# Optimization experiments

Measured on AMD Instinct MI355X. Metric: run time of the kernel, lower is better.

The kernel has to match this reference:

```python
import jax, jax.numpy as jnp
import numpy as np

B, N = 4, 2048
IN_F, OUT_F, H = 128, 128, 8
HD = OUT_F // H  # 16
ALPHA = 0.2       # LeakyReLU negative slope
TIME_DECAY = 0.1


def setup_inputs() -> dict:
    key = jax.random.key(0)
    k1, k2, k3, k4, k5 = jax.random.split(key, 5)
    node_features = jax.random.normal(k1, (B, N, IN_F), dtype=jnp.float32)
    adj_matrix = jax.random.randint(k2, (B, N, N), 0, 2, dtype=jnp.int32)
    time_matrix = jax.random.uniform(k3, (B, N, N), dtype=jnp.float32)
    # xavier_uniform with gain=1.414 as in the torch module
    def xavier(k, shape, fan_in, fan_out):
        bound = 1.414 * np.sqrt(6.0 / (fan_in + fan_out))
        return jax.random.uniform(k, shape, minval=-bound, maxval=bound, dtype=jnp.float32)
    W = xavier(k4, (H, IN_F, HD), IN_F, HD)
    a = xavier(k5, (H, 2 * HD, 1), 2 * HD, 1)
    return {"node_features": node_features, "adj_matrix": adj_matrix,
            "time_matrix": time_matrix, "W": W, "a": a}


def reference(node_features, adj_matrix, time_matrix, W, a):
    # time weights (eq 17): exp(-lambda * (t_max - t))
    current_time = jnp.max(time_matrix)
    time_weights = jnp.exp(-TIME_DECAY * (current_time - time_matrix))  # [B,N,N]

    # per-head projection: [B,H,N,HD]
    h = jnp.einsum('bni,hio->bhno', node_features, W)

    # decompose attention vector a = [a_src; a_dst] so we never build the
    # O(N^2 * 2*HD) concat tensor: e_ij = LeakyReLU(a_src.h_i + a_dst.h_j)
    a_src = a[:, :HD, 0]   # [H,HD]
    a_dst = a[:, HD:, 0]   # [H,HD]
    e_i = jnp.einsum('bhnd,hd->bhn', h, a_src)  # score contribution of node i
    e_j = jnp.einsum('bhnd,hd->bhn', h, a_dst)  # score contribution of node j
    e = e_i[:, :, :, None] + e_j[:, :, None, :]          # [B,H,N,N]
    e = jax.nn.leaky_relu(e, negative_slope=ALPHA)
    e = e * time_weights[:, None, :, :]

    # mask non-edges, normalize (dropout is identity in eval mode)
    mask = adj_matrix[:, None, :, :] == 0                 # [B,1->H,N,N]
    e = jnp.where(mask, -jnp.inf, e)
    attention = jax.nn.softmax(e, axis=-1)                # [B,H,N,N]

    # aggregate neighbors, merge heads, ELU
    out = jnp.einsum('bhij,bhjo->bhio', attention, h)     # [B,H,N,HD]
    out = jnp.transpose(out, (0, 2, 1, 3)).reshape(node_features.shape[0], node_features.shape[1], -1)
    return jax.nn.elu(out)
```

## Files before the change

### kernel.cpp

```cpp
#include <hip/hip_runtime.h>
#include <hip/hip_bf16.h>

#define BN    4
#define NN    2048
#define INF   128
#define HH    8
#define HD    16
#define ALPHA 0.2f
#define DECAY 0.1f

#define DLOG2E 0.14426950408889634f
#define LLOG2E 0.5287663729448977f

typedef __attribute__((ext_vector_type(8))) short short8;
typedef __attribute__((ext_vector_type(4))) float float4v;

__launch_bounds__(256, 8)
__global__ void k_setup(const float* __restrict__ x,
                        const float* __restrict__ W,
                        const float* __restrict__ a,
                        const float* __restrict__ tm,
                        unsigned* __restrict__ ct,
                        __hip_bfloat16* __restrict__ h_t,
                        float* __restrict__ es, float* __restrict__ ed) {
    if (blockIdx.x < 1024) {
        const uint4* p = (const uint4*)tm;
        const int nvec = BN * NN * NN / 4;
        int idx = blockIdx.x * 256 + threadIdx.x;
        const int stride = 1024 * 256;
        unsigned m = 0u;
        for (int i = idx; i < nvec; i += stride) {
            uint4 v = p[i];
            m = max(m, v.x); m = max(m, v.y); m = max(m, v.z); m = max(m, v.w);
        }
        float fm = __uint_as_float(m);
        #pragma unroll
        for (int o = 32; o >= 1; o >>= 1) fm = fmaxf(fm, __shfl_xor(fm, o));
        __shared__ float sm[4];
        if ((threadIdx.x & 63) == 0) sm[threadIdx.x >> 6] = fm;
        __syncthreads();
        if (threadIdx.x == 0) {
            float mm = fmaxf(fmaxf(sm[0], sm[1]), fmaxf(sm[2], sm[3]));
            atomicMax(ct, __float_as_uint(mm));
        }
    } else {
        int bid = blockIdx.x - 1024;
        int sub = threadIdx.x >> 7;
        int tt  = threadIdx.x & 127;
        int nn  = bid * 2 + sub;
        __shared__ float xs[2][INF];
        xs[sub][tt] = x[(size_t)nn * INF + tt];
        __syncthreads();
        int h = tt >> 4, d = tt & 15;
        const float* Wp = W + (h * INF) * HD + d;
        float acc = 0.f;
        #pragma unroll 16
        for (int i = 0; i < INF; i++) acc += xs[sub][i] * Wp[i * HD];
        int b = nn >> 11, n = nn & 2047;
        h_t[((size_t)((b * HH + h) * HD + d)) * NN + n] = __float2bfloat16(acc);
        float s  = acc * a[h * 2 * HD + d];
        float dd = acc * a[h * 2 * HD + HD + d];
        #pragma unroll
        for (int o = 8; o >= 1; o >>= 1) { s += __shfl_xor(s, o); dd += __shfl_xor(dd, o); }
        if (d == 0) {
            es[(b * HH + h) * NN + n] = s;
            ed[(b * HH + h) * NN + n] = dd;
        }
    }
}

__launch_bounds__(512, 4)
__global__ void k_attn(const int* __restrict__ adj,
                       const float* __restrict__ tm,
                       const __hip_bfloat16* __restrict__ h_t,
                       const float* __restrict__ es, const float* __restrict__ ed,
                       const unsigned* __restrict__ ctp,
                       float* __restrict__ out) {
    int t    = threadIdx.x;
    int w    = t >> 6;
    int lane = t & 63;
    int q    = lane >> 4;
    int im   = lane & 15;
    int bx   = blockIdx.x;
    int b    = bx >> 7;
    int i0   = (bx & 127) << 4;
    int i    = i0 + im;
    const int R = 16;

    __shared__ float tws[2][16 * 128];

    float ctv = __uint_as_float(*ctp);
    float c0  = fmaf(-DLOG2E, ctv, LLOG2E);
    float es_i = es[(b * HH + w) * NN + i];

    const float* ed_p = ed + (size_t)(b * HH + w) * NN + q * 8;
    const __hip_bfloat16* ht_p = h_t + ((size_t)((b * HH + w) * HD + im)) * NN + q * 8;

    int srow = t >> 5;
    int sblk = t & 31;
    int soff = srow * 128 + ((sblk ^ (srow & 7)) << 2);
    const int*   adj_s = adj + ((size_t)(b * NN + i0 + srow)) * NN + (sblk << 2);
    const float* tm_s  = tm  + ((size_t)(b * NN + i0 + srow)) * NN + (sblk << 2);

    int rbase = im * 128;
    int rx    = im & 7;

    union { uint4 u; short8 v; } ones;
    ones.u = make_uint4(0x3F803F80u, 0x3F803F80u, 0x3F803F80u, 0x3F803F80u);

    float4v acc  = {0.f, 0.f, 0.f, 0.f};
    float4v accl = {0.f, 0.f, 0.f, 0.f};

    int4   pa = *(const int4*)(adj_s);
    float4 pt = *(const float4*)(tm_s);
    {
        float w0 = (pa.x != 0) ? exp2f(fmaf(DLOG2E, pt.x, c0)) : 0.f;
        float w1 = (pa.y != 0) ? exp2f(fmaf(DLOG2E, pt.y, c0)) : 0.f;
        float w2 = (pa.z != 0) ? exp2f(fmaf(DLOG2E, pt.z, c0)) : 0.f;
        float w3 = (pa.w != 0) ? exp2f(fmaf(DLOG2E, pt.w, c0)) : 0.f;
        *(float4*)&tws[0][soff] = make_float4(w0, w1, w2, w3);
    }
    pa = *(const int4*)(adj_s + 128);
    pt = *(const float4*)(tm_s + 128);
    __syncthreads();

    for (int r = 0; r < R; r++) {
        int cur = r & 1;
        if (r + 1 < R) {
            float w0 = (pa.x != 0) ? exp2f(fmaf(DLOG2E, pt.x, c0)) : 0.f;
            float w1 = (pa.y != 0) ? exp2f(fmaf(DLOG2E, pt.y, c0)) : 0.f;
            float w2 = (pa.z != 0) ? exp2f(fmaf(DLOG2E, pt.z, c0)) : 0.f;
            float w3 = (pa.w != 0) ? exp2f(fmaf(DLOG2E, pt.w, c0)) : 0.f;
            *(float4*)&tws[cur ^ 1][soff] = make_float4(w0, w1, w2, w3);
            if (r + 2 < R) {
                pa = *(const int4*)(adj_s + (r + 2) * 128);
                pt = *(const float4*)(tm_s + (r + 2) * 128);
            }
        }
        #pragma unroll
        for (int c4 = 0; c4 < 4; c4++) {
            int blk0 = c4 * 8 + 2 * q;
            float4 w01 = *(const float4*)&tws[cur][rbase + ((blk0 ^ rx) << 2)];
            float4 w23 = *(const float4*)&tws[cur][rbase + (((blk0 + 1) ^ rx) << 2)];
            int jglob = r * 128 + c4 * 32;
            float4 e0 = *(const float4*)(ed_p + jglob);
            float4 e1 = *(const float4*)(ed_p + jglob + 4);
            uint4  hv = *(const uint4*)(ht_p + jglob);

            float wv[8] = {w01.x, w01.y, w01.z, w01.w, w23.x, w23.y, w23.z, w23.w};
            float ev[8] = {e0.x, e0.y, e0.z, e0.w, e1.x, e1.y, e1.z, e1.w};

            unsigned u[8];
            #pragma unroll
            for (int k = 0; k < 8; k++) {
                float s0 = es_i + ev[k];
                float sc = fmaxf(s0, ALPHA * s0);
                float pv = exp2f(sc * wv[k]);
                unsigned b16 = __float_as_uint(pv) + 0x8000u;
                u[k] = (wv[k] > 0.f) ? b16 : 0u;
            }
            union { uint4 w; short8 v; } af;
            af.w.x = __builtin_amdgcn_perm(u[1], u[0], 0x07060302u);
            af.w.y = __builtin_amdgcn_perm(u[3], u[2], 0x07060302u);
            af.w.z = __builtin_amdgcn_perm(u[5], u[4], 0x07060302u);
            af.w.w = __builtin_amdgcn_perm(u[7], u[6], 0x07060302u);

            union { uint4 u; short8 v; } bf;
            bf.u = hv;
            acc  = __builtin_amdgcn_mfma_f32_16x16x32_bf16(af.v, bf.v, acc, 0, 0, 0);
            accl = __builtin_amdgcn_mfma_f32_16x16x32_bf16(af.v, ones.v, accl, 0, 0, 0);
        }
        __syncthreads();
    }

    #pragma unroll
    for (int r = 0; r < 4; r++) {
        int row = q * 4 + r;
        float v = acc[r] / accl[r];
        v = (v > 0.f) ? v : expm1f(v);
        out[((size_t)(b * NN + i0 + row)) * (HH * HD) + w * HD + im] = v;
    }
}

extern "C" void kernel_launch(void* const* d_in, const int* in_sizes, int n_in,
                              void* d_out, int out_size, void* d_ws, size_t ws_size,
                              hipStream_t stream) {
    const float* x   = (const float*)d_in[0];
    const int*   adj = (const int*)d_in[1];
    const float* tm  = (const float*)d_in[2];
    const float* W   = (const float*)d_in[3];
    const float* a   = (const float*)d_in[4];
    float* out = (float*)d_out;

    float* wsf = (float*)d_ws;
    unsigned* ct = (unsigned*)wsf;
    float* es = wsf + 64;
    float* ed = es + BN * HH * NN;
    __hip_bfloat16* h_t = (__hip_bfloat16*)(ed + BN * HH * NN);

    hipMemsetAsync(d_ws, 0, 4, stream);
    k_setup<<<1024 + 4096, 256, 0, stream>>>(x, W, a, tm, ct, h_t, es, ed);
    k_attn <<<BN * (NN / 16), 512, 0, stream>>>(adj, tm, h_t, es, ed, ct, out);
}
```

Before: 235.7 us.

## Split attention blocks by head group, single-buffer weights, batch global loads

```diff
diff --git a/kernel.cpp b/kernel.cpp
--- a/kernel.cpp
+++ b/kernel.cpp
@@ -69,7 +69,7 @@
     }
 }
 
-__launch_bounds__(512, 4)
+__launch_bounds__(256, 4)
 __global__ void k_attn(const int* __restrict__ adj,
                        const float* __restrict__ tm,
                        const __hip_bfloat16* __restrict__ h_t,
@@ -77,30 +77,37 @@
                        const unsigned* __restrict__ ctp,
                        float* __restrict__ out) {
     int t    = threadIdx.x;
-    int w    = t >> 6;
+    int wv4  = t >> 6;
     int lane = t & 63;
     int q    = lane >> 4;
     int im   = lane & 15;
     int bx   = blockIdx.x;
-    int b    = bx >> 7;
-    int i0   = (bx & 127) << 4;
+    int b    = bx >> 9;
+    int hg   = (bx >> 8) & 1;
+    int i0   = (bx & 255) >> 1;
+    int itile = bx & 127;
+    hg = (bx >> 7) & 1;
+    b  = bx >> 8;
+    i0 = itile << 4;
+    int head = hg * 4 + wv4;
     int i    = i0 + im;
     const int R = 16;
 
-    __shared__ float tws[2][16 * 128];
+    __shared__ float tws[16 * 128];
 
     float ctv = __uint_as_float(*ctp);
     float c0  = fmaf(-DLOG2E, ctv, LLOG2E);
-    float es_i = es[(b * HH + w) * NN + i];
-
-    const float* ed_p = ed + (size_t)(b * HH + w) * NN + q * 8;
-    const __hip_bfloat16* ht_p = h_t + ((size_t)((b * HH + w) * HD + im)) * NN + q * 8;
-
-    int srow = t >> 5;
-    int sblk = t & 31;
-    int soff = srow * 128 + ((sblk ^ (srow & 7)) << 2);
-    const int*   adj_s = adj + ((size_t)(b * NN + i0 + srow)) * NN + (sblk << 2);
-    const float* tm_s  = tm  + ((size_t)(b * NN + i0 + srow)) * NN + (sblk << 2);
+    float es_i = es[(b * HH + head) * NN + i];
+
+    const float* ed_p = ed + (size_t)(b * HH + head) * NN + q * 8;
+    const __hip_bfloat16* ht_p = h_t + ((size_t)((b * HH + head) * HD + im)) * NN + q * 8;
+
+    int srow  = t >> 4;
+    int sblk0 = (t & 15) << 1;
+    int soff0 = srow * 128 + ((sblk0 ^ (srow & 7)) << 2);
+    int soff1 = srow * 128 + (((sblk0 + 1) ^ (srow & 7)) << 2);
+    const int*   adj_s = adj + ((size_t)(b * NN + i0 + srow)) * NN + (sblk0 << 2);
+    const float* tm_s  = tm  + ((size_t)(b * NN + i0 + srow)) * NN + (sblk0 << 2);
 
     int rbase = im * 128;
     int rx    = im & 7;
@@ -111,53 +118,60 @@
     float4v acc  = {0.f, 0.f, 0.f, 0.f};
     float4v accl = {0.f, 0.f, 0.f, 0.f};
 
-    int4   pa = *(const int4*)(adj_s);
-    float4 pt = *(const float4*)(tm_s);
-    {
-        float w0 = (pa.x != 0) ? exp2f(fmaf(DLOG2E, pt.x, c0)) : 0.f;
-        float w1 = (pa.y != 0) ? exp2f(fmaf(DLOG2E, pt.y, c0)) : 0.f;
-        float w2 = (pa.z != 0) ? exp2f(fmaf(DLOG2E, pt.z, c0)) : 0.f;
-        float w3 = (pa.w != 0) ? exp2f(fmaf(DLOG2E, pt.w, c0)) : 0.f;
-        *(float4*)&tws[0][soff] = make_float4(w0, w1, w2, w3);
-    }
-    pa = *(const int4*)(adj_s + 128);
-    pt = *(const float4*)(tm_s + 128);
-    __syncthreads();
+    int4   pa0 = *(const int4*)(adj_s);
+    int4   pa1 = *(const int4*)(adj_s + 4);
+    float4 pt0 = *(const float4*)(tm_s);
+    float4 pt1 = *(const float4*)(tm_s + 4);
 
     for (int r = 0; r < R; r++) {
-        int cur = r & 1;
+        float w00 = (pa0.x != 0) ? exp2f(fmaf(DLOG2E, pt0.x, c0)) : 0.f;
+        float w01_ = (pa0.y != 0) ? exp2f(fmaf(DLOG2E, pt0.y, c0)) : 0.f;
+        float w02 = (pa0.z != 0) ? exp2f(fmaf(DLOG2E, pt0.z, c0)) : 0.f;
+        float w03 = (pa0.w != 0) ? exp2f(fmaf(DLOG2E, pt0.w, c0)) : 0.f;
+        float w10 = (pa1.x != 0) ? exp2f(fmaf(DLOG2E, pt1.x, c0)) : 0.f;
+        float w11 = (pa1.y != 0) ? exp2f(fmaf(DLOG2E, pt1.y, c0)) : 0.f;
+        float w12 = (pa1.z != 0) ? exp2f(fmaf(DLOG2E, pt1.z, c0)) : 0.f;
+        float w13 = (pa1.w != 0) ? exp2f(fmaf(DLOG2E, pt1.w, c0)) : 0.f;
+
+        __syncthreads();
+        *(float4*)&tws[soff0] = make_float4(w00, w01_, w02, w03);
+        *(float4*)&tws[soff1] = make_float4(w10, w11, w12, w13);
         if (r + 1 < R) {
-            float w0 = (pa.x != 0) ? exp2f(fmaf(DLOG2E, pt.x, c0)) : 0.f;
-            float w1 = (pa.y != 0) ? exp2f(fmaf(DLOG2E, pt.y, c0)) : 0.f;
-            float w2 = (pa.z != 0) ? exp2f(fmaf(DLOG2E, pt.z, c0)) : 0.f;
-            float w3 = (pa.w != 0) ? exp2f(fmaf(DLOG2E, pt.w, c0)) : 0.f;
-            *(float4*)&tws[cur ^ 1][soff] = make_float4(w0, w1, w2, w3);
-            if (r + 2 < R) {
-                pa = *(const int4*)(adj_s + (r + 2) * 128);
-                pt = *(const float4*)(tm_s + (r + 2) * 128);
-            }
-        }
+            pa0 = *(const int4*)(adj_s + (r + 1) * 128);
+            pa1 = *(const int4*)(adj_s + (r + 1) * 128 + 4);
+            pt0 = *(const float4*)(tm_s + (r + 1) * 128);
+            pt1 = *(const float4*)(tm_s + (r + 1) * 128 + 4);
+        }
+        __syncthreads();
+
+        float4 E0[4], E1[4];
+        uint4  HV[4];
+        #pragma unroll
+        for (int c4 = 0; c4 < 4; c4++) {
+            int jg = r * 128 + c4 * 32;
+            E0[c4] = *(const float4*)(ed_p + jg);
+            E1[c4] = *(const float4*)(ed_p + jg + 4);
+            HV[c4] = *(const uint4*)(ht_p + jg);
+        }
+
         #pragma unroll
         for (int c4 = 0; c4 < 4; c4++) {
             int blk0 = c4 * 8 + 2 * q;
-            float4 w01 = *(const float4*)&tws[cur][rbase + ((blk0 ^ rx) << 2)];
-            float4 w23 = *(const float4*)&tws[cur][rbase + (((blk0 + 1) ^ rx) << 2)];
-            int jglob = r * 128 + c4 * 32;
-            float4 e0 = *(const float4*)(ed_p + jglob);
-            float4 e1 = *(const float4*)(ed_p + jglob + 4);
-            uint4  hv = *(const uint4*)(ht_p + jglob);
-
-            float wv[8] = {w01.x, w01.y, w01.z, w01.w, w23.x, w23.y, w23.z, w23.w};
-            float ev[8] = {e0.x, e0.y, e0.z, e0.w, e1.x, e1.y, e1.z, e1.w};
+            float4 wA = *(const float4*)&tws[rbase + ((blk0 ^ rx) << 2)];
+            float4 wB = *(const float4*)&tws[rbase + (((blk0 + 1) ^ rx) << 2)];
+
+            float wvv[8] = {wA.x, wA.y, wA.z, wA.w, wB.x, wB.y, wB.z, wB.w};
+            float evv[8] = {E0[c4].x, E0[c4].y, E0[c4].z, E0[c4].w,
+                            E1[c4].x, E1[c4].y, E1[c4].z, E1[c4].w};
 
             unsigned u[8];
             #pragma unroll
             for (int k = 0; k < 8; k++) {
-                float s0 = es_i + ev[k];
+                float s0 = es_i + evv[k];
                 float sc = fmaxf(s0, ALPHA * s0);
-                float pv = exp2f(sc * wv[k]);
+                float pv = exp2f(sc * wvv[k]);
                 unsigned b16 = __float_as_uint(pv) + 0x8000u;
-                u[k] = (wv[k] > 0.f) ? b16 : 0u;
+                u[k] = (wvv[k] > 0.f) ? b16 : 0u;
             }
             union { uint4 w; short8 v; } af;
             af.w.x = __builtin_amdgcn_perm(u[1], u[0], 0x07060302u);
@@ -166,11 +180,10 @@
             af.w.w = __builtin_amdgcn_perm(u[7], u[6], 0x07060302u);
 
             union { uint4 u; short8 v; } bf;
-            bf.u = hv;
+            bf.u = HV[c4];
             acc  = __builtin_amdgcn_mfma_f32_16x16x32_bf16(af.v, bf.v, acc, 0, 0, 0);
             accl = __builtin_amdgcn_mfma_f32_16x16x32_bf16(af.v, ones.v, accl, 0, 0, 0);
         }
-        __syncthreads();
     }
 
     #pragma unroll
@@ -178,7 +191,7 @@
         int row = q * 4 + r;
         float v = acc[r] / accl[r];
         v = (v > 0.f) ? v : expm1f(v);
-        out[((size_t)(b * NN + i0 + row)) * (HH * HD) + w * HD + im] = v;
+        out[((size_t)(b * NN + i0 + row)) * (HH * HD) + head * HD + im] = v;
     }
 }
 
@@ -200,5 +213,5 @@
 
     hipMemsetAsync(d_ws, 0, 4, stream);
     k_setup<<<1024 + 4096, 256, 0, stream>>>(x, W, a, tm, ct, h_t, es, ed);
-    k_attn <<<BN * (NN / 16), 512, 0, stream>>>(adj, tm, h_t, es, ed, ct, out);
+    k_attn <<<BN * 2 * (NN / 16), 256, 0, stream>>>(adj, tm, h_t, es, ed, ct, out);
 }
```

New measurement: 243.9 us. 3.5% more time.
